# Performance work log

Hardware: AMD Instinct MI355X
Metric: run time of the kernel (lower is better)

## Reference

```python
import jax, jax.numpy as jnp
import numpy as np

B, T, D_IN, D_H, F = 64, 512, 128, 512, 32


def setup_inputs() -> dict:
    key = jax.random.key(0)
    ks = jax.random.split(key, 8)
    s_in = 1.0 / np.sqrt(D_IN)
    s_h = 1.0 / np.sqrt(D_H)
    return {
        "input_sequence": jax.random.normal(ks[0], (B, T, D_IN), dtype=jnp.float32),
        "Wx0": jax.random.normal(ks[1], (D_H, D_IN), dtype=jnp.float32) * s_in,
        "b0": jnp.zeros((D_H,), dtype=jnp.float32),
        "Wh0": jax.random.normal(ks[2], (D_H, D_H), dtype=jnp.float32) * (0.8 * s_h),
        "d0": jnp.asarray(0.9, dtype=jnp.float32),
        "Wx1": jax.random.normal(ks[3], (D_H, D_H), dtype=jnp.float32) * s_h,
        "b1": jnp.zeros((D_H,), dtype=jnp.float32),
        "Wh1": jax.random.normal(ks[4], (D_H, D_H), dtype=jnp.float32) * (0.8 * s_h),
        "d1": jnp.asarray(0.9, dtype=jnp.float32),
        "Wp": jax.random.normal(ks[5], (D_IN, D_H), dtype=jnp.float32) * s_h,
        "bp": jnp.zeros((D_IN,), dtype=jnp.float32),
        "forecast_steps": F,
    }


def reference(input_sequence, Wx0, b0, Wh0, d0, Wx1, b1, Wh1, d1, Wp, bp, forecast_steps):
    batch = input_sequence.shape[0]
    hdim = Wh0.shape[0]

    def step(h0, h1, x):
        # h_t = decay * W_h h_{t-1} + W_x x_t + b ; layer 1 consumes updated h0
        h0 = d0 * (h0 @ Wh0.T) + x @ Wx0.T + b0
        h1 = d1 * (h1 @ Wh1.T) + h0 @ Wx1.T + b1
        return h0, h1

    # ---- encode context (scan over time, time-major) ----
    xs = jnp.swapaxes(input_sequence, 0, 1)  # [T, B, D_in]
    h0 = jnp.zeros((batch, hdim), dtype=input_sequence.dtype)
    h1 = jnp.zeros((batch, hdim), dtype=input_sequence.dtype)

    def enc(carry, xt):
        return step(*carry, xt), None

    (h0, h1), _ = jax.lax.scan(enc, (h0, h1), xs)

    pred0 = h1 @ Wp.T + bp  # [B, D_in]

    def dec(carry, _):
        h0, h1, p = carry
        h0, h1 = step(h0, h1, p)
        p_new = h1 @ Wp.T + bp
        return (h0, h1, p_new), p_new

    _, rest = jax.lax.scan(dec, (h0, h1, pred0), None, length=forecast_steps - 1)
    forecasts = jnp.concatenate([pred0[None], rest], axis=0)  # [F, B, D_in]
    return jnp.swapaxes(forecasts, 0, 1)  # [B, F, D_in]
```

## Files before the change

### kernel.cpp

```cpp
#include <hip/hip_runtime.h>
#include <cstddef>


typedef _Float16 f16;
typedef _Float16 f16x8 __attribute__((ext_vector_type(8)));
typedef _Float16 f16x4 __attribute__((ext_vector_type(4)));
typedef float f32x4 __attribute__((ext_vector_type(4)));

#define GRID 256
#define NCTR 32
#define LDA  136
#define ALPHAF 0.00390625f
#define RALPHAF 256.0f
#define DIN 128
#define NF 32

constexpr int SZ = 512*512;
constexpr int off_cat   = 0;
constexpr int off_catA1 = 327680;
constexpr int off_A0c   = 851968;
constexpr int off_A1c   = 1114112;
constexpr int off_Wpr   = 1376256;
constexpr int off_Wpc   = 1441792;
constexpr int off_Gr    = 1507328;
constexpr int off_Gc    = 2555904;
constexpr int off_P0    = 3604480;
constexpr int off_P1    = 5177344;
constexpr int GPr       = 6750208;
constexpr int GPc       = 7798784;
constexpr int GQr       = 8847360;
constexpr int GQc       = 9895936;
constexpr int off_Xin   = 10944512;
constexpr int BA        = 15138816;
constexpr int BB        = 17235968;
constexpr int BC        = 19333120;
constexpr int BD        = 21430272;
constexpr int off_S     = 23527424;
constexpr int off_Dc    = 25624576;
constexpr int off_Db    = 25690112;
constexpr int off_b0h   = 25952256;
constexpr int off_b1h   = 25952768;
constexpr int off_b0ah  = 25953280;
constexpr int off_b1ah  = 25953792;
constexpr int off_bph   = 25954304;
constexpr int off_bpX   = 25954432;
constexpr int off_ctr   = 25962624;

__host__ __device__ constexpr bool dynb(int off){
  return (off >= off_Gr && off < off_Xin) || (off >= BA && off < off_b0h);
}

constexpr int P0r(int s){ return off_P0 + s*524288; }
constexpr int P0c(int s){ return off_P0 + s*524288 + 262144; }
constexpr int P1r(int s){ return off_P1 + s*524288; }
constexpr int P1c(int s){ return off_P1 + s*524288 + 262144; }
constexpr int Bb(int k){ return k==0 ? off_Dc : off_Db + (k-1)*65536; }

struct Op {
  int type;
  int m_off, m_rstride, rows, cols;
  int k1, x1_off, x1_ks, x1_s1, x1_s2;
  int k2, x2_off, x2_ks, x2_s1, x2_s2;
  int add_off, add_ks, add_s1, add_s2;
  int bias_off; float scale;
  int y_off, y_ks, y_s1, y_s2;
  int yt_off, yt_rstride;
  int out32, tile_base;
};
constexpr int MAXOPS = 80, MAXG = 32;
struct Plan { Op ops[MAXOPS]; int gstart[MAXG+1]; int gtiles[MAXG]; int nops, ng; };

constexpr Op mko() {
  Op o{};
  o.type=0; o.m_off=0; o.m_rstride=512; o.rows=512; o.cols=512;
  o.k1=512; o.x1_off=0; o.x1_ks=512; o.x1_s1=64; o.x1_s2=0;
  o.k2=0; o.x2_off=0; o.x2_ks=512; o.x2_s1=64; o.x2_s2=0;
  o.add_off=-1; o.add_ks=512; o.add_s1=64; o.add_s2=0;
  o.bias_off=-1; o.scale=1.0f;
  o.y_off=-1; o.y_ks=512; o.y_s1=64; o.y_s2=0;
  o.yt_off=-1; o.yt_rstride=512; o.out32=0; o.tile_base=0;
  return o;
}
constexpr int op_ntiles(const Op& o){ return (o.rows>>7)*(o.cols>>6); }

struct Builder { Plan p{}; int nops=0, ng=0, gtile=0; };
constexpr void push(Builder& b, Op o){ o.tile_base=b.gtile; b.gtile+=op_ntiles(o); b.p.ops[b.nops++]=o; }
constexpr void endg(Builder& b){ b.p.gtiles[b.ng]=b.gtile; b.ng++; b.p.gstart[b.ng]=b.nops; b.gtile=0; }

constexpr Op SQ2(int m,int mrs,int x1c,int yc,int yr){
  Op o=mko(); o.m_off=m; o.m_rstride=mrs; o.x1_off=x1c; o.y_off=yc; o.yt_off=yr; return o; }
constexpr Op SQG(int mr,int xc,int yc,int yr){
  Op o=mko(); o.rows=1024; o.cols=1024; o.k1=1024; o.m_off=mr; o.m_rstride=1024;
  o.x1_off=xc; o.x1_ks=1024; o.y_off=yc; o.y_ks=1024; o.yt_off=yr; o.yt_rstride=1024; return o; }
constexpr Op P2S(int s){
  Op o=mko(); o.cols=4096; o.bias_off=off_b0h;
  o.k2=128; o.x2_off=off_Xin; o.x2_ks=128; o.x2_s1=512; o.x2_s2=(s-1)*64;
  o.y_off=(s&1)?BA:BB;
  if (s==1){ o.m_off=off_cat+512; o.m_rstride=640; o.k1=0; }
  else { o.m_off=off_cat; o.m_rstride=640; o.k1=512; o.x1_off=(s&1)?BB:BA; }
  return o; }
constexpr Op HS(int s){
  Op o=mko(); o.m_off=off_cat; o.m_rstride=640; o.cols=4096;
  o.k1=512; o.x1_off=(s&1)?BC:BB;
  o.k2=128; o.x2_off=off_Xin; o.x2_ks=128; o.x2_s1=512; o.x2_s2=(s-1)*64;
  o.bias_off=off_b0h; o.y_off=(s&1)?BB:BC; return o; }
constexpr Op RS(int s){
  Op o=mko(); o.cols=4096; o.bias_off=off_b1h;
  if (s==1){ o.m_off=off_catA1+512; o.m_rstride=1024; o.k1=512; o.x1_off=BB; o.y_off=BD; }
  else { o.m_off=off_catA1; o.m_rstride=1024; o.k1=512; o.x1_off=(s&1)?BA:BD;
         o.k2=512; o.x2_off=(s&1)?BB:BC; o.x2_ks=512; o.x2_s1=64; o.x2_s2=0;
         o.y_off=(s&1)?BD:BA; }
  return o; }
constexpr Op SCAN(int m,int d,int inb,int outb){
  Op o=mko(); o.m_off=m; o.cols=4096-d*64; o.x1_off=inb;
  o.add_off=inb; o.add_s2=d*64; o.y_off=outb; o.y_s2=d*64; return o; }
constexpr Op SCOPY(int d,int inb,int outb){
  Op o=mko(); o.k1=0; o.cols=d*64; o.add_off=inb; o.y_off=outb; return o; }
constexpr Op FOLDL(int m,int cols,int inb,int outb){
  Op o=mko(); o.m_off=m; o.cols=cols; o.x1_off=inb; o.x1_s1=128;
  o.add_off=inb; o.add_s1=128; o.add_s2=64; o.y_off=outb; return o; }
constexpr Op DECA(int k,int moff){
  Op o=mko(); int m=1<<k;
  o.rows=1024; o.cols=m*64; o.k1=1024; o.m_off=moff; o.m_rstride=1024;
  o.x1_off=off_S; o.x1_ks=1024; o.bias_off=Bb(k);
  o.y_off=off_S; o.y_ks=1024; o.y_s2=m*64; return o; }
constexpr Op DECB(int k,int moff){
  Op o=mko(); o.rows=1024; o.cols=64; o.k1=1024; o.m_off=moff; o.m_rstride=1024;
  o.x1_off=Bb(k); o.x1_ks=1024; o.bias_off=Bb(k);
  o.y_off=Bb(k+1); o.y_ks=1024; return o; }

constexpr Plan build_plan() {
  Builder b{}; b.p.gstart[0]=0;
  push(b, SQ2(off_cat,640,off_A0c,P0c(0),P0r(0)));
  push(b, SQ2(off_catA1,1024,off_A1c,P1c(0),P1r(0)));
  { Op o=mko(); o.m_off=off_cat+512; o.m_rstride=640; o.k1=128; o.x1_off=off_Wpc; o.x1_ks=128;
    o.y_off=off_Gc+512*1024; o.y_ks=1024; o.yt_off=off_Gr+512; o.yt_rstride=1024; push(b,o); }
  { Op o=mko(); o.m_off=off_cat+512; o.m_rstride=640; o.k1=128; o.x1_off=off_bpX; o.x1_ks=128;
    o.cols=64; o.bias_off=off_b0ah; o.scale=ALPHAF; o.y_off=off_Dc; o.y_ks=1024; push(b,o); }
  push(b, P2S(1)); endg(b);
  push(b, SQ2(P0r(0),512,P0c(0),P0c(1),P0r(1)));
  push(b, SQ2(P1r(0),512,P1c(0),P1c(1),P1r(1)));
  { Op o=mko(); o.m_off=off_catA1+512; o.m_rstride=1024; o.x1_off=off_A0c;
    o.y_off=off_Gc+512; o.y_ks=1024; o.yt_off=off_Gr+512*1024; o.yt_rstride=1024; push(b,o); }
  { Op o=mko(); o.m_off=off_catA1+512; o.m_rstride=1024; o.x1_off=off_Dc; o.x1_ks=1024;
    o.cols=64; o.bias_off=off_b1ah; o.y_off=off_Dc+512; o.y_ks=1024; push(b,o); }
  push(b, P2S(2)); endg(b);
  push(b, SQ2(P0r(1),512,P0c(1),P0c(2),P0r(2)));
  push(b, SQ2(P1r(1),512,P1c(1),P1c(2),P1r(2)));
  { Op o=mko(); o.m_off=off_catA1+512; o.m_rstride=1024; o.x1_off=off_Gc+512*1024; o.x1_ks=1024;
    o.add_off=off_A1c; o.y_off=off_Gc+512*1024+512; o.y_ks=1024;
    o.yt_off=off_Gr+512*1024+512; o.yt_rstride=1024; push(b,o); }
  push(b, P2S(3)); endg(b);
  push(b, SQ2(P0r(2),512,P0c(2),P0c(0),P0r(0)));
  push(b, SQ2(P1r(2),512,P1c(2),P1c(0),P1r(0)));
  push(b, P2S(4)); endg(b);
  push(b, SQ2(P0r(0),512,P0c(0),P0c(1),P0r(1)));
  push(b, SQ2(P1r(0),512,P1c(0),P1c(1),P1r(1)));
  push(b, P2S(5)); endg(b);
  push(b, P2S(6));
  push(b, SQG(off_Gr, off_Gc, GPc, GPr)); endg(b);
  push(b, P2S(7)); endg(b);
  push(b, P2S(8)); endg(b);
  push(b, SCAN(P0r(2), 1, BB, BA)); push(b, SCOPY(1, BB, BA)); endg(b);
  push(b, SCAN(P0r(0), 2, BA, BB)); push(b, SCOPY(2, BA, BB)); endg(b);
  push(b, SCAN(P0r(1), 4, BB, BA)); push(b, SCOPY(4, BB, BA)); endg(b);
  { Op o=mko(); o.m_off=off_cat; o.m_rstride=640; o.cols=4032; o.k1=512; o.x1_off=BA;
    o.k2=128; o.x2_off=off_Xin; o.x2_ks=128; o.x2_s1=512; o.x2_s2=512;
    o.bias_off=off_b0h; o.y_off=BB; o.y_s2=64; push(b,o); }
  { Op o=mko(); o.m_off=off_cat+512; o.m_rstride=640; o.cols=64; o.k1=0;
    o.k2=128; o.x2_off=off_Xin; o.x2_ks=128; o.x2_s1=512; o.x2_s2=0;
    o.bias_off=off_b0h; o.y_off=BB; push(b,o); }
  endg(b);
  for (int s=1; s<=7; ++s){ push(b, HS(s+1)); push(b, RS(s)); endg(b); }
  push(b, RS(8));
  { Op o=mko(); o.k1=0; o.cols=64; o.add_off=BC; o.add_s2=4032; o.scale=ALPHAF;
    o.y_off=off_S; o.y_ks=1024; push(b,o); }
  endg(b);
  push(b, FOLDL(P1r(2), 2048, BA, BB)); endg(b);
  push(b, FOLDL(P1r(0), 1024, BB, BC)); endg(b);
  { Op o=mko(); o.m_off=P1r(1); o.cols=64; o.x1_off=BC; o.x1_s2=896;
    o.add_off=BC; o.add_s2=960; o.scale=ALPHAF;
    o.y_off=off_S+512; o.y_ks=1024; push(b,o); }
  endg(b);
  push(b, DECA(0, off_Gr)); push(b, DECB(0, off_Gr)); endg(b);
  push(b, DECA(1, GPr)); push(b, DECB(1, GPr)); push(b, SQG(GPr,GPc,GQc,GQr)); endg(b);
  push(b, DECA(2, GQr)); push(b, DECB(2, GQr)); push(b, SQG(GQr,GQc,GPc,GPr)); endg(b);
  push(b, DECA(3, GPr)); push(b, DECB(3, GPr)); push(b, SQG(GPr,GPc,GQc,GQr)); endg(b);
  push(b, DECA(4, GQr)); endg(b);
  { Op o=mko(); o.m_off=off_Wpr; o.rows=128; o.cols=2048; o.x1_off=off_S+512; o.x1_ks=1024;
    o.bias_off=off_bph; o.scale=RALPHAF; o.out32=1; push(b,o); }
  endg(b);
  b.p.nops=b.nops; b.p.ng=b.ng;
  return b.p;
}
static constexpr Plan h_plan = build_plan();
__device__ __constant__ Plan d_plan = h_plan;

__device__ inline void issueA(const f16* pa, f16x8 (&ra)[8], bool cc) {
  if (cc)
    asm volatile(
      "global_load_dwordx4 %0, %8, off sc0 sc1\n\t"
      "global_load_dwordx4 %1, %8, off offset:16 sc0 sc1\n\t"
      "global_load_dwordx4 %2, %8, off offset:32 sc0 sc1\n\t"
      "global_load_dwordx4 %3, %8, off offset:48 sc0 sc1\n\t"
      "global_load_dwordx4 %4, %8, off offset:64 sc0 sc1\n\t"
      "global_load_dwordx4 %5, %8, off offset:80 sc0 sc1\n\t"
      "global_load_dwordx4 %6, %8, off offset:96 sc0 sc1\n\t"
      "global_load_dwordx4 %7, %8, off offset:112 sc0 sc1"
      : "=&v"(ra[0]), "=&v"(ra[1]), "=&v"(ra[2]), "=&v"(ra[3]),
        "=&v"(ra[4]), "=&v"(ra[5]), "=&v"(ra[6]), "=&v"(ra[7])
      : "v"(pa) : "memory");
  else
    asm volatile(
      "global_load_dwordx4 %0, %8, off\n\t"
      "global_load_dwordx4 %1, %8, off offset:16\n\t"
      "global_load_dwordx4 %2, %8, off offset:32\n\t"
      "global_load_dwordx4 %3, %8, off offset:48\n\t"
      "global_load_dwordx4 %4, %8, off offset:64\n\t"
      "global_load_dwordx4 %5, %8, off offset:80\n\t"
      "global_load_dwordx4 %6, %8, off offset:96\n\t"
      "global_load_dwordx4 %7, %8, off offset:112"
      : "=&v"(ra[0]), "=&v"(ra[1]), "=&v"(ra[2]), "=&v"(ra[3]),
        "=&v"(ra[4]), "=&v"(ra[5]), "=&v"(ra[6]), "=&v"(ra[7])
      : "v"(pa) : "memory");
}
__device__ inline void issueB(const f16* pb, f16x8 (&rb)[4], bool cc) {
  if (cc)
    asm volatile(
      "global_load_dwordx4 %0, %4, off sc0 sc1\n\t"
      "global_load_dwordx4 %1, %4, off offset:16 sc0 sc1\n\t"
      "global_load_dwordx4 %2, %4, off offset:32 sc0 sc1\n\t"
      "global_load_dwordx4 %3, %4, off offset:48 sc0 sc1"
      : "=&v"(rb[0]), "=&v"(rb[1]), "=&v"(rb[2]), "=&v"(rb[3])
      : "v"(pb) : "memory");
  else
    asm volatile(
      "global_load_dwordx4 %0, %4, off\n\t"
      "global_load_dwordx4 %1, %4, off offset:16\n\t"
      "global_load_dwordx4 %2, %4, off offset:32\n\t"
      "global_load_dwordx4 %3, %4, off offset:48"
      : "=&v"(rb[0]), "=&v"(rb[1]), "=&v"(rb[2]), "=&v"(rb[3])
      : "v"(pb) : "memory");
}
__device__ inline void issue_ld8(const f16* p, f16x4& r) {
  asm volatile("global_load_dwordx2 %0, %1, off sc0 sc1"
               : "=&v"(r) : "v"(p) : "memory");
}
__device__ inline void st8_cc(f16* p, f16x4 v) {
  asm volatile("global_store_dwordx2 %0, %1, off sc0 sc1" :: "v"(p), "v"(v) : "memory");
}
__device__ inline void st2_cc(f16* p, f16 v) {
  unsigned d = __builtin_bit_cast(unsigned short, v);
  asm volatile("global_store_short %0, %1, off sc0 sc1" :: "v"(p), "v"(d) : "memory");
}
__device__ inline unsigned ld_u32_cc(const unsigned* p) {
  unsigned r;
  asm volatile("global_load_dword %0, %1, off sc0 sc1\n\ts_waitcnt vmcnt(0)"
               : "=&v"(r) : "v"(p) : "memory");
  return r;
}
__device__ inline void st_u32_cc(unsigned* p, unsigned v) {
  asm volatile("global_store_dword %0, %1, off sc0 sc1" :: "v"(p), "v"(v) : "memory");
}

__device__ inline void grid_barrier(unsigned* ctrs, unsigned* flag, unsigned epoch) {
  __syncthreads();
  if (threadIdx.x == 0)
    __hip_atomic_fetch_add(&ctrs[(blockIdx.x & (NCTR-1))*32], 1u,
                           __ATOMIC_RELAXED, __HIP_MEMORY_SCOPE_AGENT);
  if (blockIdx.x == 0) {
    if (threadIdx.x < NCTR) {
      const unsigned tgt = epoch * (GRID / NCTR);
      while (ld_u32_cc(&ctrs[threadIdx.x*32]) < tgt)
        __builtin_amdgcn_s_sleep(2);
    }
    __syncthreads();
    if (threadIdx.x == 0) st_u32_cc(flag, epoch);
  } else if (threadIdx.x == 0) {
    while (ld_u32_cc(flag) < epoch)
      __builtin_amdgcn_s_sleep(2);
  }
  __syncthreads();
}

__device__ inline void chunk_srcs(const Op& o, const f16* w, int r0, int c0, int kc,
                                  const f16*& pa, const f16*& pb, bool& bcc) {
  const int tid = threadIdx.x;
  pa = w + o.m_off + (size_t)(r0 + (tid>>1)) * o.m_rstride + kc + (tid&1)*64;
  int C = c0 + (tid>>2);
  int xo, xks, xs1, xs2, xk;
  if (kc < o.k1) { xo=o.x1_off; xks=o.x1_ks; xs1=o.x1_s1; xs2=o.x1_s2; xk=kc; }
  else           { xo=o.x2_off; xks=o.x2_ks; xs1=o.x2_s1; xs2=o.x2_s2; xk=kc-o.k1; }
  int xcol = xs1*(C>>6) + (C&63) + xs2;
  pb = w + xo + (size_t)xcol*xks + xk + (tid&3)*32;
  bcc = dynb(xo);
}

__device__ inline void st_lds(f16* lsA, f16* lsB, const f16x8 (&ra)[8], const f16x8 (&rb)[4]) {
  const int tid = threadIdx.x;
  f16* da = lsA + (tid>>1)*LDA + (tid&1)*64;
#pragma unroll
  for (int i=0;i<8;++i) *(f16x8*)(da + i*8) = ra[i];
  f16* db = lsB + (tid>>2)*LDA + (tid&3)*32;
#pragma unroll
  for (int i=0;i<4;++i) *(f16x8*)(db + i*8) = rb[i];
}

__device__ inline void mfma_lds(const f16* lsA, const f16* lsB, f32x4 (&acc)[4][2]) {
  const int tid = threadIdx.x, lane = tid & 63, wid = tid >> 6;
  const int wr = wid & 1, wc = wid >> 1;
  const int ko = (lane >> 4) * 8, rl = lane & 15;
#pragma unroll
  for (int kb = 0; kb < 4; ++kb) {
    f16x8 a[4], bb[2];
#pragma unroll
    for (int s = 0; s < 4; ++s)
      a[s] = *(const f16x8*)(lsA + (wr*64 + s*16 + rl) * LDA + kb*32 + ko);
#pragma unroll
    for (int c = 0; c < 2; ++c)
      bb[c] = *(const f16x8*)(lsB + (wc*32 + c*16 + rl) * LDA + kb*32 + ko);
#pragma unroll
    for (int s = 0; s < 4; ++s)
#pragma unroll
      for (int c = 0; c < 2; ++c)
        acc[s][c] = __builtin_amdgcn_mfma_f32_16x16x32_f16(a[s], bb[c], acc[s][c], 0, 0, 0);
  }
}

#define CH_STEP(c_, raX, rbX)                                                  \
  do {                                                                         \
    __syncthreads();                                                           \
    if ((c_) < nch - 1) asm volatile("s_waitcnt vmcnt(12)" ::: "memory");      \
    else                asm volatile("s_waitcnt vmcnt(0)"  ::: "memory");      \
    st_lds(lsA, lsB, raX, rbX);                                                \
    __syncthreads();                                                           \
    if ((c_) + 2 < nch) {                                                      \
      chunk_srcs(o, w, r0, c0, ((c_)+2)*128, pa, pb, bcc);                     \
      issueA(pa, raX, mcc); issueB(pb, rbX, bcc);                              \
    }                                                                          \
    mfma_lds(lsA, lsB, acc);                                                   \
  } while (0)

__device__ void run_tile(const Op& o, int local, f16* w, float* out, f16* lsA, f16* lsB) {
  int nct = o.cols >> 6;
  int rg = local / nct, ct = local - rg * nct;
  int r0 = rg << 7, c0 = ct << 6;
  const bool mcc = dynb(o.m_off);
  const bool addcc = dynb(o.add_off);
  const bool biascc = dynb(o.bias_off);
  f32x4 acc[4][2];
#pragma unroll
  for (int s=0;s<4;++s)
#pragma unroll
    for (int c=0;c<2;++c) acc[s][c] = f32x4{0.f,0.f,0.f,0.f};
  int nch = (o.k1 + o.k2) >> 7;
  if (nch > 0) {
    const f16 *pa, *pb; bool bcc;
    f16x8 ra0[8], rb0[4], ra1[8], rb1[4];
    chunk_srcs(o, w, r0, c0, 0, pa, pb, bcc);
    issueA(pa, ra0, mcc); issueB(pb, rb0, bcc);
    if (nch > 1) {
      chunk_srcs(o, w, r0, c0, 128, pa, pb, bcc);
      issueA(pa, ra1, mcc); issueB(pb, rb1, bcc);
    }
    for (int c = 0; c < nch; c += 2) {
      CH_STEP(c, ra0, rb0);
      if (c + 1 < nch) CH_STEP(c+1, ra1, rb1);
    }
  }
  const int tid = threadIdx.x, lane = tid & 63, wid = tid >> 6;
  const int wr = wid & 1, wc = wid >> 1, rb2 = (lane >> 4) * 4, cl = lane & 15;
  f16x4 addv[4][2], biasv[4];
  bool pend = false;
  if (o.add_off >= 0) {
#pragma unroll
    for (int s = 0; s < 4; ++s) {
      int r = r0 + wr*64 + s*16 + rb2;
#pragma unroll
      for (int c = 0; c < 2; ++c) {
        int C = c0 + wc*32 + c*16 + cl;
        int acol = o.add_s1 * (C>>6) + (C&63) + o.add_s2;
        const f16* ap = w + o.add_off + (size_t)acol * o.add_ks + r;
        if (addcc) { issue_ld8(ap, addv[s][c]); pend = true; }
        else addv[s][c] = *(const f16x4*)ap;
      }
    }
  }
  if (o.bias_off >= 0) {
#pragma unroll
    for (int s = 0; s < 4; ++s) {
      int r = r0 + wr*64 + s*16 + rb2;
      const f16* bp2 = w + o.bias_off + r;
      if (biascc) { issue_ld8(bp2, biasv[s]); pend = true; }
      else biasv[s] = *(const f16x4*)bp2;
    }
  }
  if (pend) asm volatile("s_waitcnt vmcnt(0)" ::: "memory");
#pragma unroll
  for (int s = 0; s < 4; ++s) {
    int r = r0 + wr*64 + s*16 + rb2;
#pragma unroll
    for (int c = 0; c < 2; ++c) {
      int C = c0 + wc*32 + c*16 + cl;
      f32x4 v = acc[s][c];
      if (o.add_off >= 0) {
        v[0]+=(float)addv[s][c][0]; v[1]+=(float)addv[s][c][1];
        v[2]+=(float)addv[s][c][2]; v[3]+=(float)addv[s][c][3];
      }
      v[0]*=o.scale; v[1]*=o.scale; v[2]*=o.scale; v[3]*=o.scale;
      if (o.bias_off >= 0) {
        v[0]+=(float)biasv[s][0]; v[1]+=(float)biasv[s][1];
        v[2]+=(float)biasv[s][2]; v[3]+=(float)biasv[s][3];
      }
      if (o.y_off >= 0) {
        int ycol = o.y_s1 * (C>>6) + (C&63) + o.y_s2;
        f16* yp = w + o.y_off + (size_t)ycol * o.y_ks + r;
        f16x4 h; h[0]=(f16)v[0]; h[1]=(f16)v[1]; h[2]=(f16)v[2]; h[3]=(f16)v[3];
        st8_cc(yp, h);
      }
      if (o.yt_off >= 0) {
        f16* tp = w + o.yt_off;
        st2_cc(tp + (size_t)(r+0)*o.yt_rstride + C, (f16)v[0]);
        st2_cc(tp + (size_t)(r+1)*o.yt_rstride + C, (f16)v[1]);
        st2_cc(tp + (size_t)(r+2)*o.yt_rstride + C, (f16)v[2]);
        st2_cc(tp + (size_t)(r+3)*o.yt_rstride + C, (f16)v[3]);
      }
      if (o.out32) {
        float* op2 = out + (size_t)(C & 63) * (NF*DIN) + (size_t)(C >> 6) * DIN + r;
        op2[0]=v[0]; op2[1]=v[1]; op2[2]=v[2]; op2[3]=v[3];
      }
    }
  }
}

__global__ __launch_bounds__(256, 1) void rnn_main(f16* w, float* out) {
  __shared__ f16 lsA[128*LDA];
  __shared__ f16 lsB[64*LDA];
  unsigned* ctrs = (unsigned*)(w + off_ctr);
  unsigned* flag = ctrs + NCTR*32;
  const int wg = blockIdx.x;
  const int ng = d_plan.ng;
  for (int g = 0; g < ng; ++g) {
    int o0 = d_plan.gstart[g], o1 = d_plan.gstart[g+1];
    int gtot = d_plan.gtiles[g];
    for (int t = wg; t < gtot; t += GRID) {
      int oi = o0;
      while (oi + 1 < o1 && t >= d_plan.ops[oi+1].tile_base) ++oi;
      run_tile(d_plan.ops[oi], t - d_plan.ops[oi].tile_base, w, out, lsA, lsB);
    }
    grid_barrier(ctrs, flag, (unsigned)(g + 1));
  }
}

__global__ void rnn_prep(f16* w, const float* X, const float* Wx0, const float* b0,
    const float* Wh0, const float* d0p, const float* Wx1, const float* b1,
    const float* Wh1, const float* d1p, const float* Wp, const float* bp)
{
  const float d0 = d0p[0], d1 = d1p[0];
  const long n0=512L*640, n1=512L*1024, n2=(long)SZ, n3=(long)SZ, n4=128L*512, n5=512L*128,
             n6=(long)SZ, n7=(long)SZ, n8=32768L*128, n9=512, n10=512, n11=512, n12=512,
             n13=128, n14=64L*128, n15=2048;
  const long total = n0+n1+n2+n3+n4+n5+n6+n7+n8+n9+n10+n11+n12+n13+n14+n15;
  for (long idx = (long)blockIdx.x*blockDim.x + threadIdx.x; idx < total;
       idx += (long)gridDim.x*blockDim.x) {
    long j = idx;
    if (j < n0) { int r=(int)(j/640), c=(int)(j%640);
      w[off_cat+j] = (f16)(c<512 ? d0*Wh0[(long)r*512+c] : Wx0[(long)r*128+(c-512)]); continue; }
    j -= n0;
    if (j < n1) { int r=(int)(j>>10), c=(int)(j&1023);
      w[off_catA1+j] = (f16)(c<512 ? d1*Wh1[(long)r*512+c] : Wx1[(long)r*512+(c-512)]); continue; }
    j -= n1;
    if (j < n2) { int c=(int)(j>>9), r=(int)(j&511); w[off_A0c+j] = (f16)(d0*Wh0[(long)r*512+c]); continue; }
    j -= n2;
    if (j < n3) { int c=(int)(j>>9), r=(int)(j&511); w[off_A1c+j] = (f16)(d1*Wh1[(long)r*512+c]); continue; }
    j -= n3;
    if (j < n4) { w[off_Wpr+j] = (f16)Wp[j]; continue; }
    j -= n4;
    if (j < n5) { int c=(int)(j>>7), k=(int)(j&127); w[off_Wpc+j] = (f16)Wp[(long)k*512+c]; continue; }
    j -= n5;
    if (j < n6) { int r=(int)(j>>9), c=(int)(j&511);
      w[off_Gr + (long)r*1024 + c] = (f16)(d0*Wh0[(long)r*512+c]); continue; }
    j -= n6;
    if (j < n7) { int c=(int)(j>>9), r=(int)(j&511);
      w[off_Gc + (long)c*1024 + r] = (f16)(d0*Wh0[(long)r*512+c]); continue; }
    j -= n7;
    if (j < n8) { int col=(int)(j>>7), d=(int)(j&127); int t=col>>6, bb=col&63;
      w[off_Xin+j] = (f16)X[((long)bb<<16) + ((long)t<<7) + d]; continue; }
    j -= n8;
    if (j < n9) { w[off_b0h+j] = (f16)b0[j]; continue; }  j -= n9;
    if (j < n10){ w[off_b1h+j] = (f16)b1[j]; continue; }  j -= n10;
    if (j < n11){ w[off_b0ah+j] = (f16)(ALPHAF*b0[j]); continue; }  j -= n11;
    if (j < n12){ w[off_b1ah+j] = (f16)(ALPHAF*b1[j]); continue; }  j -= n12;
    if (j < n13){ w[off_bph+j] = (f16)bp[j]; continue; }  j -= n13;
    if (j < n14){ int k=(int)(j&127); w[off_bpX+j] = (f16)bp[k]; continue; }  j -= n14;
    ((unsigned*)(w + off_ctr))[j] = 0u;
  }
}

extern "C" void kernel_launch(void* const* d_in, const int* in_sizes, int n_in,
                              void* d_out, int out_size, void* d_ws, size_t ws_size,
                              hipStream_t stream) {
  (void)in_sizes; (void)n_in; (void)out_size; (void)ws_size;
  f16* w = (f16*)d_ws;
  hipLaunchKernelGGL(rnn_prep, dim3(2048), dim3(256), 0, stream,
      w,
      (const float*)d_in[0], (const float*)d_in[1], (const float*)d_in[2],
      (const float*)d_in[3], (const float*)d_in[4], (const float*)d_in[5],
      (const float*)d_in[6], (const float*)d_in[7], (const float*)d_in[8],
      (const float*)d_in[9], (const float*)d_in[10]);
  float* outp = (float*)d_out;
  void* kargs[] = { (void*)&w, (void*)&outp };
  hipLaunchCooperativeKernel((const void*)rnn_main, dim3(GRID), dim3(256), kargs, 0, stream);
}
```

Baseline: 661.1 us.

## Halve tile rows to 64 and launch two workgroups per CU

Output tiles shrink from 128x64 to 64x64, so each wave computes one 16-row strip across four column blocks and A staging per thread drops to four loads. LDS use is halved and launch bounds allow two blocks per CU, which lets the persistent cooperative grid grow to 512 workgroups when the occupancy query allows it. The barrier target now uses gridDim. The aim is more parallel tiles per phase of the small recurrent GEMMs to cut latency per grid-synchronised step. In exchange, the B operand is reused across fewer rows, the grid barrier has more participants, and the fallback path adds host-side occupancy queries.

```diff
diff --git a/kernel.cpp b/kernel.cpp
--- a/kernel.cpp
+++ b/kernel.cpp
@@ -7,7 +7,6 @@
 typedef _Float16 f16x4 __attribute__((ext_vector_type(4)));
 typedef float f32x4 __attribute__((ext_vector_type(4)));
 
-#define GRID 256
 #define NCTR 32
 #define LDA  136
 #define ALPHAF 0.00390625f
@@ -81,7 +80,7 @@
   o.yt_off=-1; o.yt_rstride=512; o.out32=0; o.tile_base=0;
   return o;
 }
-constexpr int op_ntiles(const Op& o){ return (o.rows>>7)*(o.cols>>6); }
+constexpr int op_ntiles(const Op& o){ return (o.rows>>6)*(o.cols>>6); }
 
 struct Builder { Plan p{}; int nops=0, ng=0, gtile=0; };
 constexpr void push(Builder& b, Op o){ o.tile_base=b.gtile; b.gtile+=op_ntiles(o); b.p.ops[b.nops++]=o; }
@@ -196,51 +195,23 @@
 static constexpr Plan h_plan = build_plan();
 __device__ __constant__ Plan d_plan = h_plan;
 
-__device__ inline void issueA(const f16* pa, f16x8 (&ra)[8], bool cc) {
-  if (cc)
-    asm volatile(
-      "global_load_dwordx4 %0, %8, off sc0 sc1\n\t"
-      "global_load_dwordx4 %1, %8, off offset:16 sc0 sc1\n\t"
-      "global_load_dwordx4 %2, %8, off offset:32 sc0 sc1\n\t"
-      "global_load_dwordx4 %3, %8, off offset:48 sc0 sc1\n\t"
-      "global_load_dwordx4 %4, %8, off offset:64 sc0 sc1\n\t"
-      "global_load_dwordx4 %5, %8, off offset:80 sc0 sc1\n\t"
-      "global_load_dwordx4 %6, %8, off offset:96 sc0 sc1\n\t"
-      "global_load_dwordx4 %7, %8, off offset:112 sc0 sc1"
-      : "=&v"(ra[0]), "=&v"(ra[1]), "=&v"(ra[2]), "=&v"(ra[3]),
-        "=&v"(ra[4]), "=&v"(ra[5]), "=&v"(ra[6]), "=&v"(ra[7])
-      : "v"(pa) : "memory");
-  else
-    asm volatile(
-      "global_load_dwordx4 %0, %8, off\n\t"
-      "global_load_dwordx4 %1, %8, off offset:16\n\t"
-      "global_load_dwordx4 %2, %8, off offset:32\n\t"
-      "global_load_dwordx4 %3, %8, off offset:48\n\t"
-      "global_load_dwordx4 %4, %8, off offset:64\n\t"
-      "global_load_dwordx4 %5, %8, off offset:80\n\t"
-      "global_load_dwordx4 %6, %8, off offset:96\n\t"
-      "global_load_dwordx4 %7, %8, off offset:112"
-      : "=&v"(ra[0]), "=&v"(ra[1]), "=&v"(ra[2]), "=&v"(ra[3]),
-        "=&v"(ra[4]), "=&v"(ra[5]), "=&v"(ra[6]), "=&v"(ra[7])
-      : "v"(pa) : "memory");
-}
-__device__ inline void issueB(const f16* pb, f16x8 (&rb)[4], bool cc) {
+__device__ inline void issue4(const f16* p, f16x8 (&r)[4], bool cc) {
   if (cc)
     asm volatile(
       "global_load_dwordx4 %0, %4, off sc0 sc1\n\t"
       "global_load_dwordx4 %1, %4, off offset:16 sc0 sc1\n\t"
       "global_load_dwordx4 %2, %4, off offset:32 sc0 sc1\n\t"
       "global_load_dwordx4 %3, %4, off offset:48 sc0 sc1"
-      : "=&v"(rb[0]), "=&v"(rb[1]), "=&v"(rb[2]), "=&v"(rb[3])
-      : "v"(pb) : "memory");
+      : "=&v"(r[0]), "=&v"(r[1]), "=&v"(r[2]), "=&v"(r[3])
+      : "v"(p) : "memory");
   else
     asm volatile(
       "global_load_dwordx4 %0, %4, off\n\t"
       "global_load_dwordx4 %1, %4, off offset:16\n\t"
       "global_load_dwordx4 %2, %4, off offset:32\n\t"
       "global_load_dwordx4 %3, %4, off offset:48"
-      : "=&v"(rb[0]), "=&v"(rb[1]), "=&v"(rb[2]), "=&v"(rb[3])
-      : "v"(pb) : "memory");
+      : "=&v"(r[0]), "=&v"(r[1]), "=&v"(r[2]), "=&v"(r[3])
+      : "v"(p) : "memory");
 }
 __device__ inline void issue_ld8(const f16* p, f16x4& r) {
   asm volatile("global_load_dwordx2 %0, %1, off sc0 sc1"
@@ -270,7 +241,7 @@
                            __ATOMIC_RELAXED, __HIP_MEMORY_SCOPE_AGENT);
   if (blockIdx.x == 0) {
     if (threadIdx.x < NCTR) {
-      const unsigned tgt = epoch * (GRID / NCTR);
+      const unsigned tgt = epoch * (gridDim.x / NCTR);
       while (ld_u32_cc(&ctrs[threadIdx.x*32]) < tgt)
         __builtin_amdgcn_s_sleep(2);
     }
@@ -286,7 +257,7 @@
 __device__ inline void chunk_srcs(const Op& o, const f16* w, int r0, int c0, int kc,
                                   const f16*& pa, const f16*& pb, bool& bcc) {
   const int tid = threadIdx.x;
-  pa = w + o.m_off + (size_t)(r0 + (tid>>1)) * o.m_rstride + kc + (tid&1)*64;
+  pa = w + o.m_off + (size_t)(r0 + (tid>>2)) * o.m_rstride + kc + (tid&3)*32;
   int C = c0 + (tid>>2);
   int xo, xks, xs1, xs2, xk;
   if (kc < o.k1) { xo=o.x1_off; xks=o.x1_ks; xs1=o.x1_s1; xs2=o.x1_s2; xk=kc; }
@@ -296,47 +267,40 @@
   bcc = dynb(xo);
 }
 
-__device__ inline void st_lds(f16* lsA, f16* lsB, const f16x8 (&ra)[8], const f16x8 (&rb)[4]) {
+__device__ inline void st_lds(f16* lsA, f16* lsB, const f16x8 (&ra)[4], const f16x8 (&rb)[4]) {
   const int tid = threadIdx.x;
-  f16* da = lsA + (tid>>1)*LDA + (tid&1)*64;
-#pragma unroll
-  for (int i=0;i<8;++i) *(f16x8*)(da + i*8) = ra[i];
+  f16* da = lsA + (tid>>2)*LDA + (tid&3)*32;
+#pragma unroll
+  for (int i=0;i<4;++i) *(f16x8*)(da + i*8) = ra[i];
   f16* db = lsB + (tid>>2)*LDA + (tid&3)*32;
 #pragma unroll
   for (int i=0;i<4;++i) *(f16x8*)(db + i*8) = rb[i];
 }
 
-__device__ inline void mfma_lds(const f16* lsA, const f16* lsB, f32x4 (&acc)[4][2]) {
+__device__ inline void mfma_lds(const f16* lsA, const f16* lsB, f32x4 (&acc)[4]) {
   const int tid = threadIdx.x, lane = tid & 63, wid = tid >> 6;
-  const int wr = wid & 1, wc = wid >> 1;
   const int ko = (lane >> 4) * 8, rl = lane & 15;
 #pragma unroll
   for (int kb = 0; kb < 4; ++kb) {
-    f16x8 a[4], bb[2];
-#pragma unroll
-    for (int s = 0; s < 4; ++s)
-      a[s] = *(const f16x8*)(lsA + (wr*64 + s*16 + rl) * LDA + kb*32 + ko);
-#pragma unroll
-    for (int c = 0; c < 2; ++c)
-      bb[c] = *(const f16x8*)(lsB + (wc*32 + c*16 + rl) * LDA + kb*32 + ko);
-#pragma unroll
-    for (int s = 0; s < 4; ++s)
-#pragma unroll
-      for (int c = 0; c < 2; ++c)
-        acc[s][c] = __builtin_amdgcn_mfma_f32_16x16x32_f16(a[s], bb[c], acc[s][c], 0, 0, 0);
+    f16x8 a = *(const f16x8*)(lsA + (wid*16 + rl) * LDA + kb*32 + ko);
+#pragma unroll
+    for (int n = 0; n < 4; ++n) {
+      f16x8 bb = *(const f16x8*)(lsB + (n*16 + rl) * LDA + kb*32 + ko);
+      acc[n] = __builtin_amdgcn_mfma_f32_16x16x32_f16(a, bb, acc[n], 0, 0, 0);
+    }
   }
 }
 
 #define CH_STEP(c_, raX, rbX)                                                  \
   do {                                                                         \
     __syncthreads();                                                           \
-    if ((c_) < nch - 1) asm volatile("s_waitcnt vmcnt(12)" ::: "memory");      \
-    else                asm volatile("s_waitcnt vmcnt(0)"  ::: "memory");      \
+    if ((c_) < nch - 1) asm volatile("s_waitcnt vmcnt(8)" ::: "memory");       \
+    else                asm volatile("s_waitcnt vmcnt(0)" ::: "memory");       \
     st_lds(lsA, lsB, raX, rbX);                                                \
     __syncthreads();                                                           \
     if ((c_) + 2 < nch) {                                                      \
       chunk_srcs(o, w, r0, c0, ((c_)+2)*128, pa, pb, bcc);                     \
-      issueA(pa, raX, mcc); issueB(pb, rbX, bcc);                              \
+      issue4(pa, raX, mcc); issue4(pb, rbX, bcc);                              \
     }                                                                          \
     mfma_lds(lsA, lsB, acc);                                                   \
   } while (0)
@@ -344,24 +308,22 @@
 __device__ void run_tile(const Op& o, int local, f16* w, float* out, f16* lsA, f16* lsB) {
   int nct = o.cols >> 6;
   int rg = local / nct, ct = local - rg * nct;
-  int r0 = rg << 7, c0 = ct << 6;
+  int r0 = rg << 6, c0 = ct << 6;
   const bool mcc = dynb(o.m_off);
   const bool addcc = dynb(o.add_off);
   const bool biascc = dynb(o.bias_off);
-  f32x4 acc[4][2];
-#pragma unroll
-  for (int s=0;s<4;++s)
-#pragma unroll
-    for (int c=0;c<2;++c) acc[s][c] = f32x4{0.f,0.f,0.f,0.f};
+  f32x4 acc[4];
+#pragma unroll
+  for (int n=0;n<4;++n) acc[n] = f32x4{0.f,0.f,0.f,0.f};
   int nch = (o.k1 + o.k2) >> 7;
   if (nch > 0) {
     const f16 *pa, *pb; bool bcc;
-    f16x8 ra0[8], rb0[4], ra1[8], rb1[4];
+    f16x8 ra0[4], rb0[4], ra1[4], rb1[4];
     chunk_srcs(o, w, r0, c0, 0, pa, pb, bcc);
-    issueA(pa, ra0, mcc); issueB(pb, rb0, bcc);
+    issue4(pa, ra0, mcc); issue4(pb, rb0, bcc);
     if (nch > 1) {
       chunk_srcs(o, w, r0, c0, 128, pa, pb, bcc);
-      issueA(pa, ra1, mcc); issueB(pb, rb1, bcc);
+      issue4(pa, ra1, mcc); issue4(pb, rb1, bcc);
     }
     for (int c = 0; c < nch; c += 2) {
       CH_STEP(c, ra0, rb0);
@@ -369,81 +331,71 @@
     }
   }
   const int tid = threadIdx.x, lane = tid & 63, wid = tid >> 6;
-  const int wr = wid & 1, wc = wid >> 1, rb2 = (lane >> 4) * 4, cl = lane & 15;
-  f16x4 addv[4][2], biasv[4];
+  const int q4 = (lane >> 4) * 4, cl = lane & 15;
+  const int r = r0 + wid*16 + q4;
+  f16x4 addv[4], biasv;
   bool pend = false;
   if (o.add_off >= 0) {
 #pragma unroll
-    for (int s = 0; s < 4; ++s) {
-      int r = r0 + wr*64 + s*16 + rb2;
-#pragma unroll
-      for (int c = 0; c < 2; ++c) {
-        int C = c0 + wc*32 + c*16 + cl;
-        int acol = o.add_s1 * (C>>6) + (C&63) + o.add_s2;
-        const f16* ap = w + o.add_off + (size_t)acol * o.add_ks + r;
-        if (addcc) { issue_ld8(ap, addv[s][c]); pend = true; }
-        else addv[s][c] = *(const f16x4*)ap;
-      }
+    for (int n = 0; n < 4; ++n) {
+      int C = c0 + n*16 + cl;
+      int acol = o.add_s1 * (C>>6) + (C&63) + o.add_s2;
+      const f16* ap = w + o.add_off + (size_t)acol * o.add_ks + r;
+      if (addcc) { issue_ld8(ap, addv[n]); pend = true; }
+      else addv[n] = *(const f16x4*)ap;
     }
   }
   if (o.bias_off >= 0) {
-#pragma unroll
-    for (int s = 0; s < 4; ++s) {
-      int r = r0 + wr*64 + s*16 + rb2;
-      const f16* bp2 = w + o.bias_off + r;
-      if (biascc) { issue_ld8(bp2, biasv[s]); pend = true; }
-      else biasv[s] = *(const f16x4*)bp2;
-    }
+    const f16* bp2 = w + o.bias_off + r;
+    if (biascc) { issue_ld8(bp2, biasv); pend = true; }
+    else biasv = *(const f16x4*)bp2;
   }
   if (pend) asm volatile("s_waitcnt vmcnt(0)" ::: "memory");
 #pragma unroll
-  for (int s = 0; s < 4; ++s) {
-    int r = r0 + wr*64 + s*16 + rb2;
-#pragma unroll
-    for (int c = 0; c < 2; ++c) {
-      int C = c0 + wc*32 + c*16 + cl;
-      f32x4 v = acc[s][c];
-      if (o.add_off >= 0) {
-        v[0]+=(float)addv[s][c][0]; v[1]+=(float)addv[s][c][1];
-        v[2]+=(float)addv[s][c][2]; v[3]+=(float)addv[s][c][3];
-      }
-      v[0]*=o.scale; v[1]*=o.scale; v[2]*=o.scale; v[3]*=o.scale;
-      if (o.bias_off >= 0) {
-        v[0]+=(float)biasv[s][0]; v[1]+=(float)biasv[s][1];
-        v[2]+=(float)biasv[s][2]; v[3]+=(float)biasv[s][3];
-      }
-      if (o.y_off >= 0) {
-        int ycol = o.y_s1 * (C>>6) + (C&63) + o.y_s2;
-        f16* yp = w + o.y_off + (size_t)ycol * o.y_ks + r;
-        f16x4 h; h[0]=(f16)v[0]; h[1]=(f16)v[1]; h[2]=(f16)v[2]; h[3]=(f16)v[3];
-        st8_cc(yp, h);
-      }
-      if (o.yt_off >= 0) {
-        f16* tp = w + o.yt_off;
-        st2_cc(tp + (size_t)(r+0)*o.yt_rstride + C, (f16)v[0]);
-        st2_cc(tp + (size_t)(r+1)*o.yt_rstride + C, (f16)v[1]);
-        st2_cc(tp + (size_t)(r+2)*o.yt_rstride + C, (f16)v[2]);
-        st2_cc(tp + (size_t)(r+3)*o.yt_rstride + C, (f16)v[3]);
-      }
-      if (o.out32) {
-        float* op2 = out + (size_t)(C & 63) * (NF*DIN) + (size_t)(C >> 6) * DIN + r;
-        op2[0]=v[0]; op2[1]=v[1]; op2[2]=v[2]; op2[3]=v[3];
-      }
-    }
-  }
-}
-
-__global__ __launch_bounds__(256, 1) void rnn_main(f16* w, float* out) {
-  __shared__ f16 lsA[128*LDA];
+  for (int n = 0; n < 4; ++n) {
+    int C = c0 + n*16 + cl;
+    f32x4 v = acc[n];
+    if (o.add_off >= 0) {
+      v[0]+=(float)addv[n][0]; v[1]+=(float)addv[n][1];
+      v[2]+=(float)addv[n][2]; v[3]+=(float)addv[n][3];
+    }
+    v[0]*=o.scale; v[1]*=o.scale; v[2]*=o.scale; v[3]*=o.scale;
+    if (o.bias_off >= 0) {
+      v[0]+=(float)biasv[0]; v[1]+=(float)biasv[1];
+      v[2]+=(float)biasv[2]; v[3]+=(float)biasv[3];
+    }
+    if (o.y_off >= 0) {
+      int ycol = o.y_s1 * (C>>6) + (C&63) + o.y_s2;
+      f16* yp = w + o.y_off + (size_t)ycol * o.y_ks + r;
+      f16x4 h; h[0]=(f16)v[0]; h[1]=(f16)v[1]; h[2]=(f16)v[2]; h[3]=(f16)v[3];
+      st8_cc(yp, h);
+    }
+    if (o.yt_off >= 0) {
+      f16* tp = w + o.yt_off;
+      st2_cc(tp + (size_t)(r+0)*o.yt_rstride + C, (f16)v[0]);
+      st2_cc(tp + (size_t)(r+1)*o.yt_rstride + C, (f16)v[1]);
+      st2_cc(tp + (size_t)(r+2)*o.yt_rstride + C, (f16)v[2]);
+      st2_cc(tp + (size_t)(r+3)*o.yt_rstride + C, (f16)v[3]);
+    }
+    if (o.out32) {
+      float* op2 = out + (size_t)(C & 63) * (NF*DIN) + (size_t)(C >> 6) * DIN + r;
+      op2[0]=v[0]; op2[1]=v[1]; op2[2]=v[2]; op2[3]=v[3];
+    }
+  }
+}
+
+__global__ __launch_bounds__(256, 2) void rnn_main(f16* w, float* out) {
+  __shared__ f16 lsA[64*LDA];
   __shared__ f16 lsB[64*LDA];
   unsigned* ctrs = (unsigned*)(w + off_ctr);
   unsigned* flag = ctrs + NCTR*32;
   const int wg = blockIdx.x;
+  const int stride = gridDim.x;
   const int ng = d_plan.ng;
   for (int g = 0; g < ng; ++g) {
     int o0 = d_plan.gstart[g], o1 = d_plan.gstart[g+1];
     int gtot = d_plan.gtiles[g];
-    for (int t = wg; t < gtot; t += GRID) {
+    for (int t = wg; t < gtot; t += stride) {
       int oi = o0;
       while (oi + 1 < o1 && t >= d_plan.ops[oi+1].tile_base) ++oi;
       run_tile(d_plan.ops[oi], t - d_plan.ops[oi].tile_base, w, out, lsA, lsB);
@@ -510,5 +462,14 @@
       (const float*)d_in[9], (const float*)d_in[10]);
   float* outp = (float*)d_out;
   void* kargs[] = { (void*)&w, (void*)&outp };
-  hipLaunchCooperativeKernel((const void*)rnn_main, dim3(GRID), dim3(256), kargs, 0, stream);
-}
+  int nb = 0;
+  hipError_t qe = hipOccupancyMaxActiveBlocksPerMultiprocessor(
+      &nb, (const void*)rnn_main, 256, 0);
+  int grid = (qe == hipSuccess && nb >= 2) ? 512 : 256;
+  hipError_t le = hipLaunchCooperativeKernel((const void*)rnn_main, dim3(grid),
+                                             dim3(256), kargs, 0, stream);
+  if (le != hipSuccess && grid == 512) {
+    hipLaunchCooperativeKernel((const void*)rnn_main, dim3(256),
+                               dim3(256), kargs, 0, stream);
+  }
+}
```

Result: faster. 553.9 us (-16.2%).
